# Optimization experiments

Measured on AMD Instinct MI355X. Metric: run time of the kernel, lower is better.

The kernel has to match this reference:

```python
import jax, jax.numpy as jnp
import numpy as np

IP = 10  # power-iteration steps


def setup_inputs() -> dict:
    key = jax.random.key(0)
    k1, k2 = jax.random.split(key)
    B, C, H, W = 16, 512, 64, 64
    x = jax.random.normal(k1, (B, C, H, W), dtype=jnp.float32)
    # random start vector for power iteration (torch: FloatTensor.normal_(0,1))
    v = jax.random.normal(k2, (B, C, 1), dtype=jnp.float32)
    return {"x": x, "v": v}


def reference(x, v):
    B, C, H, W = x.shape
    # w = x.view(B,C,HW).permute(0,2,1) -> (B, HW, C)
    w = jnp.transpose(x.reshape(B, C, H * W), (0, 2, 1))
    # W_s = w^T w : (B, C, C)
    Ws = jnp.einsum('bnc,bnd->bcd', w, w)

    def step(vc, _):
        vc = jnp.matmul(Ws, vc)                                   # (B,C,1)
        vc = vc / jnp.linalg.norm(vc, axis=(1, 2), keepdims=True)  # per-batch L2 norm
        return vc, None

    v, _ = jax.lax.scan(step, v, None, length=IP)
    # u = W v, normalized : (B, HW, 1)
    u = jnp.matmul(w, v)
    u = u / jnp.linalg.norm(u, axis=(1, 2), keepdims=True)
    # z = u v^T : (B, HW, C) -> (B, C, H, W)
    z = jnp.matmul(u, jnp.transpose(v, (0, 2, 1)))
    z = jnp.transpose(z, (0, 2, 1)).reshape(B, C, H, W)
    return x + z
```

## Files before the change

### kernel.cpp

```cpp
#include <hip/hip_runtime.h>
#include <stdint.h>

#define NB 16
#define NC 512
#define NHW 4096

typedef unsigned short u16;
typedef __bf16 bf16x8 __attribute__((ext_vector_type(8)));
typedef float f32x4 __attribute__((ext_vector_type(4)));
typedef unsigned short u16x8 __attribute__((ext_vector_type(8)));
typedef unsigned short u16x4 __attribute__((ext_vector_type(4)));

#define AS1 __attribute__((address_space(1)))
#define AS3 __attribute__((address_space(3)))

__device__ __forceinline__ float bf2f(u16 h) {
    union { unsigned u; float f; } a; a.u = ((unsigned)h) << 16; return a.f;
}
__device__ __forceinline__ u16 f2bf(float f) {
    union { float f; unsigned u; } a; a.f = f;
    unsigned u = a.u;
    return (u16)((u + 0x7FFFu + ((u >> 16) & 1u)) >> 16);
}

__global__ __launch_bounds__(256) void k_to_bf16(const float* __restrict__ x,
                                                 u16* __restrict__ xb) {
    int i = blockIdx.x * 256 + threadIdx.x;
    f32x4 v = ((const f32x4*)x)[i];
    u16x4 o;
    o[0] = f2bf(v[0]); o[1] = f2bf(v[1]); o[2] = f2bf(v[2]); o[3] = f2bf(v[3]);
    ((u16x4*)xb)[i] = o;
}

__global__ __launch_bounds__(256, 2)
void k_gemm_bt(const u16* __restrict__ Ab, const u16* __restrict__ Bb,
               u16* __restrict__ Cb, int K, int N,
               size_t sA, size_t sB, size_t sC, float scale) {
    __shared__ u16 As[128 * 32];
    __shared__ u16 Bs[128 * 32];
    const int tid = threadIdx.x;
    const int wave = tid >> 6, lane = tid & 63;
    const int b = blockIdx.z;
    const u16* A  = Ab + (size_t)b * sA + (size_t)blockIdx.x * 128 * K;
    const u16* Bm = Bb + (size_t)b * sB + (size_t)blockIdx.y * 128 * K;

    const int srow = tid >> 2;
    const int scol = (tid & 3) * 8;
    const u16* ag0 = A  + (size_t)srow * K + scol;
    const u16* ag1 = ag0 + (size_t)64 * K;
    const u16* bg0 = Bm + (size_t)srow * K + scol;
    const u16* bg1 = bg0 + (size_t)64 * K;
    u16* asw0 = &As[wave * 512];
    u16* asw1 = &As[2048 + wave * 512];
    u16* bsw0 = &Bs[wave * 512];
    u16* bsw1 = &Bs[2048 + wave * 512];

    f32x4 acc[4][4];
#pragma unroll
    for (int i = 0; i < 4; i++)
#pragma unroll
        for (int j = 0; j < 4; j++) acc[i][j] = f32x4{0.f, 0.f, 0.f, 0.f};

    const int rm = (wave & 1) * 64;
    const int rn = (wave >> 1) * 64;
    const int m16 = lane & 15, quad = lane >> 4;

    for (int k0 = 0; k0 < K; k0 += 32) {
        __syncthreads();
        __builtin_amdgcn_global_load_lds((AS1 void*)(ag0 + k0), (AS3 void*)asw0, 16, 0, 0);
        __builtin_amdgcn_global_load_lds((AS1 void*)(ag1 + k0), (AS3 void*)asw1, 16, 0, 0);
        __builtin_amdgcn_global_load_lds((AS1 void*)(bg0 + k0), (AS3 void*)bsw0, 16, 0, 0);
        __builtin_amdgcn_global_load_lds((AS1 void*)(bg1 + k0), (AS3 void*)bsw1, 16, 0, 0);
        __syncthreads();

        bf16x8 af[4], bfr[4];
#pragma unroll
        for (int mi = 0; mi < 4; mi++)
            af[mi] = *(const bf16x8*)&As[(rm + mi * 16 + m16) * 32 + quad * 8];
#pragma unroll
        for (int ni = 0; ni < 4; ni++)
            bfr[ni] = *(const bf16x8*)&Bs[(rn + ni * 16 + m16) * 32 + quad * 8];
#pragma unroll
        for (int mi = 0; mi < 4; mi++)
#pragma unroll
            for (int ni = 0; ni < 4; ni++)
                acc[mi][ni] = __builtin_amdgcn_mfma_f32_16x16x32_bf16(
                    af[mi], bfr[ni], acc[mi][ni], 0, 0, 0);
    }

    u16* Co = Cb + (size_t)b * sC + ((size_t)blockIdx.x * 128) * N + blockIdx.y * 128;
    const int rq = quad * 4;
#pragma unroll
    for (int mi = 0; mi < 4; mi++)
#pragma unroll
        for (int ni = 0; ni < 4; ni++)
#pragma unroll
            for (int r = 0; r < 4; r++) {
                int row = rm + mi * 16 + rq + r;
                int col = rn + ni * 16 + m16;
                Co[(size_t)row * N + col] = f2bf(acc[mi][ni][r] * scale);
            }
}

__device__ __forceinline__ float block_sum(float x, float* red, int tid) {
#pragma unroll
    for (int o = 32; o > 0; o >>= 1) x += __shfl_down(x, o, 64);
    __syncthreads();
    if ((tid & 63) == 0) red[tid >> 6] = x;
    __syncthreads();
    float s = red[0];
#pragma unroll
    for (int w = 1; w < 8; w++) s += red[w];
    return s;
}

__global__ __launch_bounds__(512, 1)
void k_power_iter(const u16* __restrict__ S, const u16* __restrict__ S2,
                  const float* __restrict__ v0, float* __restrict__ vhat,
                  float* __restrict__ coef) {
    const int b = blockIdx.x, tid = threadIdx.x;
    __shared__ float va[NC], vb[NC];
    __shared__ float red[16];
    const u16* Sb  = S  + (size_t)b * NC * NC;
    const u16* S2b = S2 + (size_t)b * NC * NC;
    va[tid] = v0[b * NC + tid];
    __syncthreads();
    float* cur = va;
    float* nxt = vb;
    for (int it = 0; it < 5; ++it) {
        const u16* row = S2b + (size_t)tid * NC;
        float acc = 0.f;
        for (int k = 0; k < NC; k += 8) {
            u16x8 w = *(const u16x8*)(row + k);
#pragma unroll
            for (int j = 0; j < 8; j++) acc += bf2f(w[j]) * cur[k + j];
        }
        nxt[tid] = acc;
        __syncthreads();
        float* t = cur; cur = nxt; nxt = t;
    }
    const u16* row = Sb + (size_t)tid * NC;
    float r = 0.f;
    for (int k = 0; k < NC; k += 8) {
        u16x8 w = *(const u16x8*)(row + k);
#pragma unroll
        for (int j = 0; j < 8; j++) r += bf2f(w[j]) * cur[k + j];
    }
    float myv = cur[tid];
    float n10 = block_sum(myv * myv, red, tid);
    float d   = block_sum(myv * r, red, tid);
    float inv = rsqrtf(n10);
    float s   = sqrtf(4096.f * d / n10);
    float vh  = myv * inv;
    vhat[b * NC + tid] = vh;
    coef[b * NC + tid] = vh / s;
}

__global__ __launch_bounds__(256)
void k_compute_t(const u16* __restrict__ xb, const float* __restrict__ vhat,
                 float* __restrict__ tp) {
    const int b = blockIdx.z, cc = blockIdx.y, nc = blockIdx.x, tid = threadIdx.x;
    __shared__ float vsh[128];
    if (tid < 128) vsh[tid] = vhat[b * NC + cc * 128 + tid];
    __syncthreads();
    const int n0 = nc * 2048 + tid * 8;
    const u16* xp = xb + (size_t)b * NC * NHW + (size_t)cc * 128 * NHW + n0;
    float acc[8] = {0.f, 0.f, 0.f, 0.f, 0.f, 0.f, 0.f, 0.f};
    for (int c = 0; c < 128; c++) {
        u16x8 w = *(const u16x8*)xp;
        xp += NHW;
        float vc = vsh[c];
#pragma unroll
        for (int j = 0; j < 8; j++) acc[j] += bf2f(w[j]) * vc;
    }
    float* dst = tp + (size_t)(b * 4 + cc) * NHW + n0;
    *(f32x4*)dst       = f32x4{acc[0], acc[1], acc[2], acc[3]};
    *(f32x4*)(dst + 4) = f32x4{acc[4], acc[5], acc[6], acc[7]};
}

__global__ __launch_bounds__(256)
void k_epilogue(const float* __restrict__ x, const float* __restrict__ tp,
                const float* __restrict__ coef, float* __restrict__ out) {
    const int b = blockIdx.z, cc = blockIdx.y, nc = blockIdx.x, tid = threadIdx.x;
    __shared__ float tl[1024];
    __shared__ float cf[64];
    const int nbase = nc * 1024, cbase = cc * 64;
    for (int i = tid; i < 1024; i += 256) {
        float s = 0.f;
#pragma unroll
        for (int p = 0; p < 4; p++) s += tp[(size_t)(b * 4 + p) * NHW + nbase + i];
        tl[i] = s;
    }
    if (tid < 64) cf[tid] = coef[b * NC + cbase + tid];
    __syncthreads();
    f32x4 tv = ((const f32x4*)tl)[tid];
    for (int rr = 0; rr < 64; rr++) {
        size_t off = ((size_t)(b * NC + cbase + rr)) * NHW + nbase + tid * 4;
        f32x4 xv = *(const f32x4*)(x + off);
        float c = cf[rr];
        f32x4 o = xv + tv * c;
        *(f32x4*)(out + off) = o;
    }
}

extern "C" void kernel_launch(void* const* d_in, const int* in_sizes, int n_in,
                              void* d_out, int out_size, void* d_ws, size_t ws_size,
                              hipStream_t stream) {
    const float* x  = (const float*)d_in[0];
    const float* v0 = (const float*)d_in[1];
    float* out = (float*)d_out;

    char* ws = (char*)d_ws;
    u16* xb    = (u16*)ws;
    u16* S     = (u16*)(ws + 67108864);
    u16* S2    = (u16*)(ws + 67108864 + 8388608);
    float* vhat = (float*)(ws + 83886080);
    float* coef = (float*)(ws + 83886080 + 32768);
    float* tp   = (float*)(ws + 83886080 + 65536);

    k_to_bf16<<<dim3(32768), dim3(256), 0, stream>>>(x, xb);
    k_gemm_bt<<<dim3(4, 4, NB), dim3(256), 0, stream>>>(
        xb, xb, S, NHW, NC, (size_t)NC * NHW, (size_t)NC * NHW, (size_t)NC * NC,
        1.f / 4096.f);
    k_gemm_bt<<<dim3(4, 4, NB), dim3(256), 0, stream>>>(
        S, S, S2, NC, NC, (size_t)NC * NC, (size_t)NC * NC, (size_t)NC * NC, 1.f);
    k_power_iter<<<dim3(NB), dim3(512), 0, stream>>>(S, S2, v0, vhat, coef);
    k_compute_t<<<dim3(2, 4, NB), dim3(256), 0, stream>>>(xb, vhat, tp);
    k_epilogue<<<dim3(4, 8, NB), dim3(256), 0, stream>>>(x, tp, coef, out);
}
```

Before: 470.9 us.

## Restructure power-iteration matvec to wave-per-row coalesced loads with 1024 threads

```diff
diff --git a/kernel.cpp b/kernel.cpp
--- a/kernel.cpp
+++ b/kernel.cpp
@@ -102,58 +102,84 @@
             }
 }
 
-__device__ __forceinline__ float block_sum(float x, float* red, int tid) {
+__device__ __forceinline__ float block_sum16(float x, float* red, int tid) {
 #pragma unroll
     for (int o = 32; o > 0; o >>= 1) x += __shfl_down(x, o, 64);
-    __syncthreads();
     if ((tid & 63) == 0) red[tid >> 6] = x;
     __syncthreads();
     float s = red[0];
 #pragma unroll
-    for (int w = 1; w < 8; w++) s += red[w];
+    for (int w = 1; w < 16; w++) s += red[w];
+    __syncthreads();
     return s;
 }
 
-__global__ __launch_bounds__(512, 1)
+__global__ __launch_bounds__(1024, 1)
 void k_power_iter(const u16* __restrict__ S, const u16* __restrict__ S2,
                   const float* __restrict__ v0, float* __restrict__ vhat,
                   float* __restrict__ coef) {
     const int b = blockIdx.x, tid = threadIdx.x;
+    const int wave = tid >> 6, lane = tid & 63;
     __shared__ float va[NC], vb[NC];
     __shared__ float red[16];
     const u16* Sb  = S  + (size_t)b * NC * NC;
     const u16* S2b = S2 + (size_t)b * NC * NC;
-    va[tid] = v0[b * NC + tid];
+    if (tid < NC) va[tid] = v0[b * NC + tid];
     __syncthreads();
     float* cur = va;
     float* nxt = vb;
+
+    const int row0 = wave * 32;
     for (int it = 0; it < 5; ++it) {
-        const u16* row = S2b + (size_t)tid * NC;
-        float acc = 0.f;
-        for (int k = 0; k < NC; k += 8) {
-            u16x8 w = *(const u16x8*)(row + k);
-#pragma unroll
-            for (int j = 0; j < 8; j++) acc += bf2f(w[j]) * cur[k + j];
+        float c[8];
+#pragma unroll
+        for (int j = 0; j < 8; j++) c[j] = cur[lane * 8 + j];
+        const u16* M0 = S2b + (size_t)row0 * NC + lane * 8;
+#pragma unroll 4
+        for (int rr = 0; rr < 32; ++rr) {
+            u16x8 m = *(const u16x8*)(M0 + (size_t)rr * NC);
+            float d0 = bf2f(m[0]) * c[0] + bf2f(m[1]) * c[1];
+            float d1 = bf2f(m[2]) * c[2] + bf2f(m[3]) * c[3];
+            float d2 = bf2f(m[4]) * c[4] + bf2f(m[5]) * c[5];
+            float d3 = bf2f(m[6]) * c[6] + bf2f(m[7]) * c[7];
+            float d = (d0 + d1) + (d2 + d3);
+#pragma unroll
+            for (int o = 32; o > 0; o >>= 1) d += __shfl_down(d, o, 64);
+            if (lane == 0) nxt[row0 + rr] = d;
         }
-        nxt[tid] = acc;
         __syncthreads();
         float* t = cur; cur = nxt; nxt = t;
     }
-    const u16* row = Sb + (size_t)tid * NC;
-    float r = 0.f;
-    for (int k = 0; k < NC; k += 8) {
-        u16x8 w = *(const u16x8*)(row + k);
-#pragma unroll
-        for (int j = 0; j < 8; j++) r += bf2f(w[j]) * cur[k + j];
-    }
-    float myv = cur[tid];
-    float n10 = block_sum(myv * myv, red, tid);
-    float d   = block_sum(myv * r, red, tid);
+    {
+        float c[8];
+#pragma unroll
+        for (int j = 0; j < 8; j++) c[j] = cur[lane * 8 + j];
+        const u16* M0 = Sb + (size_t)row0 * NC + lane * 8;
+#pragma unroll 4
+        for (int rr = 0; rr < 32; ++rr) {
+            u16x8 m = *(const u16x8*)(M0 + (size_t)rr * NC);
+            float d0 = bf2f(m[0]) * c[0] + bf2f(m[1]) * c[1];
+            float d1 = bf2f(m[2]) * c[2] + bf2f(m[3]) * c[3];
+            float d2 = bf2f(m[4]) * c[4] + bf2f(m[5]) * c[5];
+            float d3 = bf2f(m[6]) * c[6] + bf2f(m[7]) * c[7];
+            float d = (d0 + d1) + (d2 + d3);
+#pragma unroll
+            for (int o = 32; o > 0; o >>= 1) d += __shfl_down(d, o, 64);
+            if (lane == 0) nxt[row0 + rr] = d;
+        }
+        __syncthreads();
+    }
+    float myv = (tid < NC) ? cur[tid] : 0.f;
+    float myr = (tid < NC) ? nxt[tid] : 0.f;
+    float n10 = block_sum16(myv * myv, red, tid);
+    float d   = block_sum16(myv * myr, red, tid);
     float inv = rsqrtf(n10);
     float s   = sqrtf(4096.f * d / n10);
-    float vh  = myv * inv;
-    vhat[b * NC + tid] = vh;
-    coef[b * NC + tid] = vh / s;
+    if (tid < NC) {
+        float vh = myv * inv;
+        vhat[b * NC + tid] = vh;
+        coef[b * NC + tid] = vh / s;
+    }
 }
 
 __global__ __launch_bounds__(256)
@@ -224,7 +250,7 @@
         1.f / 4096.f);
     k_gemm_bt<<<dim3(4, 4, NB), dim3(256), 0, stream>>>(
         S, S, S2, NC, NC, (size_t)NC * NC, (size_t)NC * NC, (size_t)NC * NC, 1.f);
-    k_power_iter<<<dim3(NB), dim3(512), 0, stream>>>(S, S2, v0, vhat, coef);
+    k_power_iter<<<dim3(NB), dim3(1024), 0, stream>>>(S, S2, v0, vhat, coef);
     k_compute_t<<<dim3(2, 4, NB), dim3(256), 0, stream>>>(xb, vhat, tp);
     k_epilogue<<<dim3(4, 8, NB), dim3(256), 0, stream>>>(x, tp, coef, out);
 }
```

Measured after the change: 457.0 us. 2.9% less time.

## Parallelize power-iteration matvec over 1024 threads and compute u-norm directly

Applied to the files above, without the earlier changes.

```diff
diff --git a/kernel.cpp b/kernel.cpp
--- a/kernel.cpp
+++ b/kernel.cpp
@@ -102,58 +102,70 @@
             }
 }
 
-__device__ __forceinline__ float block_sum(float x, float* red, int tid) {
-#pragma unroll
-    for (int o = 32; o > 0; o >>= 1) x += __shfl_down(x, o, 64);
-    __syncthreads();
-    if ((tid & 63) == 0) red[tid >> 6] = x;
-    __syncthreads();
-    float s = red[0];
-#pragma unroll
-    for (int w = 1; w < 8; w++) s += red[w];
-    return s;
-}
-
-__global__ __launch_bounds__(512, 1)
-void k_power_iter(const u16* __restrict__ S, const u16* __restrict__ S2,
-                  const float* __restrict__ v0, float* __restrict__ vhat,
-                  float* __restrict__ coef) {
+__global__ __launch_bounds__(1024, 1)
+void k_power_iter(const u16* __restrict__ S2, const float* __restrict__ v0,
+                  float* __restrict__ vhat) {
     const int b = blockIdx.x, tid = threadIdx.x;
     __shared__ float va[NC], vb[NC];
+    __shared__ float part[NC][16];
     __shared__ float red[16];
-    const u16* Sb  = S  + (size_t)b * NC * NC;
-    const u16* S2b = S2 + (size_t)b * NC * NC;
-    va[tid] = v0[b * NC + tid];
-    __syncthreads();
+    const u16* Mb = S2 + (size_t)b * NC * NC;
+    const int cg = tid & 15;
+    const int r0 = tid >> 4;
+    if (tid < NC) va[tid] = v0[b * NC + tid];
     float* cur = va;
     float* nxt = vb;
+    __syncthreads();
+
     for (int it = 0; it < 5; ++it) {
-        const u16* row = S2b + (size_t)tid * NC;
-        float acc = 0.f;
-        for (int k = 0; k < NC; k += 8) {
-            u16x8 w = *(const u16x8*)(row + k);
-#pragma unroll
-            for (int j = 0; j < 8; j++) acc += bf2f(w[j]) * cur[k + j];
+        float c[4][8];
+#pragma unroll
+        for (int p = 0; p < 4; p++) {
+            f32x4 lo = *(const f32x4*)&cur[cg * 8 + p * 128];
+            f32x4 hi = *(const f32x4*)&cur[cg * 8 + p * 128 + 4];
+            c[p][0] = lo[0]; c[p][1] = lo[1]; c[p][2] = lo[2]; c[p][3] = lo[3];
+            c[p][4] = hi[0]; c[p][5] = hi[1]; c[p][6] = hi[2]; c[p][7] = hi[3];
         }
-        nxt[tid] = acc;
+#pragma unroll 2
+        for (int pass = 0; pass < 8; ++pass) {
+            const int r = pass * 64 + r0;
+            const u16* row = Mb + (size_t)r * NC + cg * 8;
+            u16x8 m[4];
+#pragma unroll
+            for (int p = 0; p < 4; p++) m[p] = *(const u16x8*)(row + p * 128);
+            float a0 = 0.f, a1 = 0.f, a2 = 0.f, a3 = 0.f;
+#pragma unroll
+            for (int j = 0; j < 8; j++) {
+                a0 += bf2f(m[0][j]) * c[0][j];
+                a1 += bf2f(m[1][j]) * c[1][j];
+                a2 += bf2f(m[2][j]) * c[2][j];
+                a3 += bf2f(m[3][j]) * c[3][j];
+            }
+            part[r][cg] = (a0 + a1) + (a2 + a3);
+        }
+        __syncthreads();
+        if (tid < NC) {
+            f32x4 s0 = *(const f32x4*)&part[tid][0];
+            f32x4 s1 = *(const f32x4*)&part[tid][4];
+            f32x4 s2 = *(const f32x4*)&part[tid][8];
+            f32x4 s3 = *(const f32x4*)&part[tid][12];
+            f32x4 s = (s0 + s1) + (s2 + s3);
+            nxt[tid] = (s[0] + s[1]) + (s[2] + s[3]);
+        }
         __syncthreads();
         float* t = cur; cur = nxt; nxt = t;
     }
-    const u16* row = Sb + (size_t)tid * NC;
-    float r = 0.f;
-    for (int k = 0; k < NC; k += 8) {
-        u16x8 w = *(const u16x8*)(row + k);
-#pragma unroll
-        for (int j = 0; j < 8; j++) r += bf2f(w[j]) * cur[k + j];
-    }
-    float myv = cur[tid];
-    float n10 = block_sum(myv * myv, red, tid);
-    float d   = block_sum(myv * r, red, tid);
-    float inv = rsqrtf(n10);
-    float s   = sqrtf(4096.f * d / n10);
-    float vh  = myv * inv;
-    vhat[b * NC + tid] = vh;
-    coef[b * NC + tid] = vh / s;
+
+    float mv = (tid < NC) ? cur[tid] : 0.f;
+    float x = mv * mv;
+#pragma unroll
+    for (int o = 32; o > 0; o >>= 1) x += __shfl_down(x, o, 64);
+    if ((tid & 63) == 0) red[tid >> 6] = x;
+    __syncthreads();
+    float n = red[0];
+#pragma unroll
+    for (int w = 1; w < 16; w++) n += red[w];
+    if (tid < NC) vhat[b * NC + tid] = mv * rsqrtf(n);
 }
 
 __global__ __launch_bounds__(256)
@@ -178,20 +190,42 @@
     *(f32x4*)(dst + 4) = f32x4{acc[4], acc[5], acc[6], acc[7]};
 }
 
+__global__ __launch_bounds__(1024, 1)
+void k_tnorm(const float* __restrict__ tp, float* __restrict__ tsum,
+             float* __restrict__ sinv) {
+    const int b = blockIdx.x, tid = threadIdx.x;
+    __shared__ float red[16];
+    const int n0 = tid * 4;
+    f32x4 s = f32x4{0.f, 0.f, 0.f, 0.f};
+#pragma unroll
+    for (int p = 0; p < 4; p++)
+        s += *(const f32x4*)(tp + (size_t)(b * 4 + p) * NHW + n0);
+    *(f32x4*)(tsum + (size_t)b * NHW + n0) = s;
+    float ss = s[0] * s[0] + s[1] * s[1] + s[2] * s[2] + s[3] * s[3];
+#pragma unroll
+    for (int o = 32; o > 0; o >>= 1) ss += __shfl_down(ss, o, 64);
+    if ((tid & 63) == 0) red[tid >> 6] = ss;
+    __syncthreads();
+    if (tid == 0) {
+        float n = red[0];
+#pragma unroll
+        for (int w = 1; w < 16; w++) n += red[w];
+        sinv[b] = rsqrtf(n);
+    }
+}
+
 __global__ __launch_bounds__(256)
-void k_epilogue(const float* __restrict__ x, const float* __restrict__ tp,
-                const float* __restrict__ coef, float* __restrict__ out) {
+void k_epilogue(const float* __restrict__ x, const float* __restrict__ tsum,
+                const float* __restrict__ vhat, const float* __restrict__ sinv,
+                float* __restrict__ out) {
     const int b = blockIdx.z, cc = blockIdx.y, nc = blockIdx.x, tid = threadIdx.x;
     __shared__ float tl[1024];
     __shared__ float cf[64];
     const int nbase = nc * 1024, cbase = cc * 64;
-    for (int i = tid; i < 1024; i += 256) {
-        float s = 0.f;
-#pragma unroll
-        for (int p = 0; p < 4; p++) s += tp[(size_t)(b * 4 + p) * NHW + nbase + i];
-        tl[i] = s;
-    }
-    if (tid < 64) cf[tid] = coef[b * NC + cbase + tid];
+    const float si = sinv[b];
+    for (int i = tid; i < 1024; i += 256)
+        tl[i] = tsum[(size_t)b * NHW + nbase + i];
+    if (tid < 64) cf[tid] = vhat[b * NC + cbase + tid] * si;
     __syncthreads();
     f32x4 tv = ((const f32x4*)tl)[tid];
     for (int rr = 0; rr < 64; rr++) {
@@ -211,12 +245,13 @@
     float* out = (float*)d_out;
 
     char* ws = (char*)d_ws;
-    u16* xb    = (u16*)ws;
-    u16* S     = (u16*)(ws + 67108864);
-    u16* S2    = (u16*)(ws + 67108864 + 8388608);
+    u16* xb     = (u16*)ws;
+    u16* S      = (u16*)(ws + 67108864);
+    u16* S2     = (u16*)(ws + 67108864 + 8388608);
     float* vhat = (float*)(ws + 83886080);
-    float* coef = (float*)(ws + 83886080 + 32768);
     float* tp   = (float*)(ws + 83886080 + 65536);
+    float* tsum = (float*)(ws + 83886080 + 65536 + 1048576);
+    float* sinv = (float*)(ws + 83886080 + 65536 + 1048576 + 262144);
 
     k_to_bf16<<<dim3(32768), dim3(256), 0, stream>>>(x, xb);
     k_gemm_bt<<<dim3(4, 4, NB), dim3(256), 0, stream>>>(
@@ -224,7 +259,8 @@
         1.f / 4096.f);
     k_gemm_bt<<<dim3(4, 4, NB), dim3(256), 0, stream>>>(
         S, S, S2, NC, NC, (size_t)NC * NC, (size_t)NC * NC, (size_t)NC * NC, 1.f);
-    k_power_iter<<<dim3(NB), dim3(512), 0, stream>>>(S, S2, v0, vhat, coef);
+    k_power_iter<<<dim3(NB), dim3(1024), 0, stream>>>(S2, v0, vhat);
     k_compute_t<<<dim3(2, 4, NB), dim3(256), 0, stream>>>(xb, vhat, tp);
-    k_epilogue<<<dim3(4, 8, NB), dim3(256), 0, stream>>>(x, tp, coef, out);
-}
+    k_tnorm<<<dim3(NB), dim3(1024), 0, stream>>>(tp, tsum, sinv);
+    k_epilogue<<<dim3(4, 8, NB), dim3(256), 0, stream>>>(x, tsum, vhat, sinv, out);
+}
```

Result: faster. 400.6 us (-14.9%).
